# Kernel optimization log

Hardware: AMD Instinct MI355X
Metric: run time of the kernel (lower is better)

Reference implementation:

```python
import jax, jax.numpy as jnp
import numpy as np

EPS = 1e-5

def _layernorm(x, g, b):
    mu = jnp.mean(x, axis=-1, keepdims=True)
    var = jnp.mean(jnp.square(x - mu), axis=-1, keepdims=True)
    return (x - mu) * jax.lax.rsqrt(var + EPS) * g + b

def _orthogonal(key, out_dim, in_dim):
    a = jax.random.normal(key, (max(out_dim, in_dim), min(out_dim, in_dim)), dtype=jnp.float32)
    q, r = jnp.linalg.qr(a)
    q = q * jnp.sign(jnp.diagonal(r))
    if out_dim < in_dim:
        q = q.T
    return q  # [out_dim, in_dim]

def setup_inputs() -> dict:
    key = jax.random.key(0)
    ks = jax.random.split(key, 4)
    B, OBS, H1, H2, F = 262144, 512, 128, 128, 128
    obs = jax.random.normal(ks[0], (B, OBS), dtype=jnp.float32)
    return {
        "obs": obs,
        "w1": _orthogonal(ks[1], H1, OBS), "b1": jnp.zeros((H1,), jnp.float32),
        "g1": jnp.ones((H1,), jnp.float32), "be1": jnp.zeros((H1,), jnp.float32),
        "w2": _orthogonal(ks[2], H2, H1), "b2": jnp.zeros((H2,), jnp.float32),
        "g2": jnp.ones((H2,), jnp.float32), "be2": jnp.zeros((H2,), jnp.float32),
        "w3": _orthogonal(ks[3], F, H2), "b3": jnp.zeros((F,), jnp.float32),
    }

def reference(obs, w1, b1, g1, be1, w2, b2, g2, be2, w3, b3):
    x = jnp.tanh(_layernorm(obs @ w1.T + b1, g1, be1))
    x = jnp.tanh(_layernorm(x @ w2.T + b2, g2, be2))
    return jnp.tanh(x @ w3.T + b3)
```

## Files before the change

kernel.cpp:

```cpp
#include <hip/hip_runtime.h>
#include <hip/hip_bf16.h>

typedef __attribute__((ext_vector_type(8))) __bf16 bf16x8;
typedef __attribute__((ext_vector_type(4))) float f32x4;
typedef __attribute__((ext_vector_type(8))) float f32x8;

static __device__ __forceinline__ unsigned short bf16r(float f) {
  unsigned u = __builtin_bit_cast(unsigned, f);
  return (unsigned short)((u + 0x7FFFu + ((u >> 16) & 1u)) >> 16);
}

static __device__ __forceinline__ float ftanh(float x) {
  float e = __builtin_amdgcn_exp2f(x * 2.8853900817779268f);
  return 1.0f - 2.0f * __builtin_amdgcn_rcpf(e + 1.0f);
}

static __device__ __forceinline__ void gload_lds16(const void* g, void* l) {
  __builtin_amdgcn_global_load_lds(
      (const __attribute__((address_space(1))) unsigned int*)g,
      (__attribute__((address_space(3))) unsigned int*)l, 16, 0, 0);
}

__global__ void pack_kernel(const float* __restrict__ w1, const float* __restrict__ w2,
                            const float* __restrict__ w3, const float* __restrict__ b1,
                            const float* __restrict__ g1, const float* __restrict__ be1,
                            const float* __restrict__ b2, const float* __restrict__ g2,
                            const float* __restrict__ be2, const float* __restrict__ b3,
                            unsigned short* __restrict__ w1pk, unsigned short* __restrict__ w2pk,
                            unsigned short* __restrict__ w3pk, float* __restrict__ ppk) {
  int idx = blockIdx.x * 256 + threadIdx.x;
  if (idx < 65536) {
    int j = idx & 7, l = (idx >> 3) & 63, s = (idx >> 9) & 15, t = idx >> 13;
    int row = t * 16 + (l & 15);
    int col = s * 32 + (l >> 4) * 8 + j;
    w1pk[idx] = bf16r(w1[row * 512 + col]);
  } else if (idx < 81920) {
    int i = idx - 65536;
    int j = i & 7, l = (i >> 3) & 63, s = (i >> 9) & 3, t = i >> 11;
    int row = t * 16 + (l & 15);
    int col = (2 * s + (j >> 2)) * 16 + (l >> 4) * 4 + (j & 3);
    w2pk[i] = bf16r(w2[row * 128 + col]);
  } else if (idx < 98304) {
    int i = idx - 81920;
    int j = i & 7, l = (i >> 3) & 63, s = (i >> 9) & 3, t = i >> 11;
    int row = t * 16 + (l & 15);
    int col = (2 * s + (j >> 2)) * 16 + (l >> 4) * 4 + (j & 3);
    w3pk[i] = bf16r(w3[row * 128 + col]);
  } else if (idx < 99200) {
    int i = idx - 98304;
    int p = i >> 7;
    int r = i & 127;
    int qq = r >> 5, ii = r & 31;
    int m = (ii >> 2) * 16 + qq * 4 + (ii & 3);
    const float* src = (p == 0) ? b1 : (p == 1) ? g1 : (p == 2) ? be1
                     : (p == 3) ? b2 : (p == 4) ? g2 : (p == 5) ? be2 : b3;
    ppk[i] = src[m];
  }
}

__global__ __launch_bounds__(1024)
__attribute__((amdgpu_waves_per_eu(4, 4)))
void backbone_main(const float* __restrict__ obs,
                   const unsigned char* __restrict__ w1pk_g,
                   const bf16x8* __restrict__ w2pk,
                   const bf16x8* __restrict__ w3pk,
                   const float* __restrict__ ppk,
                   float* __restrict__ out) {
  __shared__ __align__(16) unsigned char lds[131072];

  const int tid  = threadIdx.x;
  const int lane = tid & 63;
  const int wv   = tid >> 6;
  const int q    = lane >> 4;
  const int rl   = lane & 15;
  const int l8   = lane >> 3;
  const int c8   = lane & 7;
  const unsigned rowR = blockIdx.x * 256 + wv * 16;
  const size_t brow = (size_t)rowR + (unsigned)rl;

  const unsigned char* gsrc = (const unsigned char*)obs
      + ((size_t)rowR + (unsigned)l8) * 2048 + (unsigned)((c8 ^ l8) * 16);
  unsigned char* obsS = lds + 65536 + wv * 4096;

  const unsigned rd0 = (unsigned)(rl * 128 + ((2 * q) ^ (rl & 7)) * 16);
  const unsigned rd1 = (unsigned)(rl * 128 + ((2 * q + 1) ^ (rl & 7)) * 16);

  gload_lds16(gsrc,                 obsS);
  gload_lds16(gsrc + 16384,         obsS + 1024);
  gload_lds16(gsrc + 128,           obsS + 2048);
  gload_lds16(gsrc + 128 + 16384,   obsS + 3072);
#pragma unroll
  for (int r = 0; r < 4; ++r) {
    unsigned o = r * 16384 + tid * 16;
    gload_lds16(w1pk_g + o + (o >> 13) * 8192, lds + r * 16384 + wv * 1024);
  }
  __syncthreads();

  const bf16x8* w1l = (const bf16x8*)lds;

  f32x4 acc[8];
#pragma unroll
  for (int t = 0; t < 8; ++t) acc[t] = (f32x4){0.f, 0.f, 0.f, 0.f};

#define KSTEP(s, WAITSTR)                                                        \
  {                                                                              \
    asm volatile("s_waitcnt " WAITSTR ::: "memory");                             \
    __builtin_amdgcn_sched_barrier(0);                                           \
    unsigned char* slot = obsS + ((s) & 1) * 2048;                               \
    f32x4 r0 = *(const f32x4*)(slot + rd0);                                      \
    f32x4 r1 = *(const f32x4*)(slot + rd1);                                      \
    asm volatile("s_waitcnt lgkmcnt(0)" ::: "memory");                           \
    __builtin_amdgcn_sched_barrier(0);                                           \
    if ((s) + 2 <= 15) {                                                         \
      gload_lds16(gsrc + ((s) + 2) * 128,         slot);                         \
      gload_lds16(gsrc + ((s) + 2) * 128 + 16384, slot + 1024);                  \
    }                                                                            \
    f32x8 rr = {r0.x, r0.y, r0.z, r0.w, r1.x, r1.y, r1.z, r1.w};                 \
    bf16x8 bfrag = __builtin_convertvector(rr, bf16x8);                          \
    _Pragma("unroll")                                                            \
    for (int t = 0; t < 8; ++t) {                                                \
      bf16x8 af = w1l[(t * 8 + ((s) & 7)) * 64 + lane];                          \
      acc[t] = __builtin_amdgcn_mfma_f32_16x16x32_bf16(af, bfrag, acc[t], 0, 0, 0); \
    }                                                                            \
  }

  KSTEP(0, "vmcnt(2)")
  KSTEP(1, "vmcnt(2)")
  KSTEP(2, "vmcnt(2)")
  KSTEP(3, "vmcnt(2)")
  KSTEP(4, "vmcnt(2)")
  KSTEP(5, "vmcnt(2)")
  KSTEP(6, "vmcnt(2)")
  KSTEP(7, "vmcnt(2)")

  __syncthreads();
#pragma unroll
  for (int r = 0; r < 4; ++r) {
    unsigned o = r * 16384 + tid * 16;
    gload_lds16(w1pk_g + o + ((o >> 13) + 1) * 8192, lds + r * 16384 + wv * 1024);
  }
  __syncthreads();

  KSTEP(8,  "vmcnt(2)")
  KSTEP(9,  "vmcnt(2)")
  KSTEP(10, "vmcnt(2)")
  KSTEP(11, "vmcnt(2)")
  KSTEP(12, "vmcnt(2)")
  KSTEP(13, "vmcnt(2)")
  KSTEP(14, "vmcnt(2)")
  KSTEP(15, "vmcnt(0)")
#undef KSTEP

  bf16x8 pkv[4];

  {
    const float* pb = ppk + 0 * 128 + q * 32;
    const float* pg = ppk + 1 * 128 + q * 32;
    const float* pe = ppk + 2 * 128 + q * 32;
    float s1 = 0.f, s2 = 0.f;
#pragma unroll
    for (int t = 0; t < 8; ++t) {
      f32x4 bb = *(const f32x4*)(pb + t * 4);
      f32x4 v = acc[t];
      v.x += bb.x; v.y += bb.y; v.z += bb.z; v.w += bb.w;
      acc[t] = v;
      s1 += (v.x + v.y) + (v.z + v.w);
      s2 += (v.x * v.x + v.y * v.y) + (v.z * v.z + v.w * v.w);
    }
    s1 += __shfl_xor(s1, 16, 64);
    s1 += __shfl_xor(s1, 32, 64);
    s2 += __shfl_xor(s2, 16, 64);
    s2 += __shfl_xor(s2, 32, 64);
    float mu  = s1 * (1.0f / 128.0f);
    float var = s2 * (1.0f / 128.0f) - mu * mu;
    float rs  = __builtin_amdgcn_rsqf(var + 1e-5f);
#pragma unroll
    for (int t2 = 0; t2 < 4; ++t2) {
      f32x4 ga = *(const f32x4*)(pg + (2 * t2) * 4);
      f32x4 gb = *(const f32x4*)(pg + (2 * t2 + 1) * 4);
      f32x4 ea = *(const f32x4*)(pe + (2 * t2) * 4);
      f32x4 eb = *(const f32x4*)(pe + (2 * t2 + 1) * 4);
      f32x4 va = acc[2 * t2];
      f32x4 vb = acc[2 * t2 + 1];
      f32x8 cat = {ftanh((va.x - mu) * rs * ga.x + ea.x),
                   ftanh((va.y - mu) * rs * ga.y + ea.y),
                   ftanh((va.z - mu) * rs * ga.z + ea.z),
                   ftanh((va.w - mu) * rs * ga.w + ea.w),
                   ftanh((vb.x - mu) * rs * gb.x + eb.x),
                   ftanh((vb.y - mu) * rs * gb.y + eb.y),
                   ftanh((vb.z - mu) * rs * gb.z + eb.z),
                   ftanh((vb.w - mu) * rs * gb.w + eb.w)};
      pkv[t2] = __builtin_convertvector(cat, bf16x8);
    }
  }

#pragma unroll
  for (int t = 0; t < 8; ++t) acc[t] = (f32x4){0.f, 0.f, 0.f, 0.f};
#pragma unroll
  for (int s = 0; s < 4; ++s) {
#pragma unroll
    for (int t = 0; t < 8; ++t) {
      bf16x8 af = w2pk[(t * 4 + s) * 64 + lane];
      acc[t] = __builtin_amdgcn_mfma_f32_16x16x32_bf16(af, pkv[s], acc[t], 0, 0, 0);
    }
  }

  {
    const float* pb = ppk + 3 * 128 + q * 32;
    const float* pg = ppk + 4 * 128 + q * 32;
    const float* pe = ppk + 5 * 128 + q * 32;
    float s1 = 0.f, s2 = 0.f;
#pragma unroll
    for (int t = 0; t < 8; ++t) {
      f32x4 bb = *(const f32x4*)(pb + t * 4);
      f32x4 v = acc[t];
      v.x += bb.x; v.y += bb.y; v.z += bb.z; v.w += bb.w;
      acc[t] = v;
      s1 += (v.x + v.y) + (v.z + v.w);
      s2 += (v.x * v.x + v.y * v.y) + (v.z * v.z + v.w * v.w);
    }
    s1 += __shfl_xor(s1, 16, 64);
    s1 += __shfl_xor(s1, 32, 64);
    s2 += __shfl_xor(s2, 16, 64);
    s2 += __shfl_xor(s2, 32, 64);
    float mu  = s1 * (1.0f / 128.0f);
    float var = s2 * (1.0f / 128.0f) - mu * mu;
    float rs  = __builtin_amdgcn_rsqf(var + 1e-5f);
#pragma unroll
    for (int t2 = 0; t2 < 4; ++t2) {
      f32x4 ga = *(const f32x4*)(pg + (2 * t2) * 4);
      f32x4 gb = *(const f32x4*)(pg + (2 * t2 + 1) * 4);
      f32x4 ea = *(const f32x4*)(pe + (2 * t2) * 4);
      f32x4 eb = *(const f32x4*)(pe + (2 * t2 + 1) * 4);
      f32x4 va = acc[2 * t2];
      f32x4 vb = acc[2 * t2 + 1];
      f32x8 cat = {ftanh((va.x - mu) * rs * ga.x + ea.x),
                   ftanh((va.y - mu) * rs * ga.y + ea.y),
                   ftanh((va.z - mu) * rs * ga.z + ea.z),
                   ftanh((va.w - mu) * rs * ga.w + ea.w),
                   ftanh((vb.x - mu) * rs * gb.x + eb.x),
                   ftanh((vb.y - mu) * rs * gb.y + eb.y),
                   ftanh((vb.z - mu) * rs * gb.z + eb.z),
                   ftanh((vb.w - mu) * rs * gb.w + eb.w)};
      pkv[t2] = __builtin_convertvector(cat, bf16x8);
    }
  }

#pragma unroll
  for (int t = 0; t < 8; ++t) acc[t] = (f32x4){0.f, 0.f, 0.f, 0.f};
#pragma unroll
  for (int s = 0; s < 4; ++s) {
#pragma unroll
    for (int t = 0; t < 8; ++t) {
      bf16x8 af = w3pk[(t * 4 + s) * 64 + lane];
      acc[t] = __builtin_amdgcn_mfma_f32_16x16x32_bf16(af, pkv[s], acc[t], 0, 0, 0);
    }
  }

  {
    const float* pb = ppk + 6 * 128 + q * 32;
    float* orow = out + brow * 128 + q * 4;
#pragma unroll
    for (int t = 0; t < 8; ++t) {
      f32x4 bb = *(const f32x4*)(pb + t * 4);
      f32x4 v = acc[t];
      f32x4 o = {ftanh(v.x + bb.x), ftanh(v.y + bb.y),
                 ftanh(v.z + bb.z), ftanh(v.w + bb.w)};
      __builtin_nontemporal_store(o, (f32x4*)(orow + t * 16));
    }
  }
}

extern "C" void kernel_launch(void* const* d_in, const int* in_sizes, int n_in,
                              void* d_out, int out_size, void* d_ws, size_t ws_size,
                              hipStream_t stream) {
  const float* obs = (const float*)d_in[0];
  const float* w1  = (const float*)d_in[1];
  const float* b1  = (const float*)d_in[2];
  const float* g1  = (const float*)d_in[3];
  const float* be1 = (const float*)d_in[4];
  const float* w2  = (const float*)d_in[5];
  const float* b2  = (const float*)d_in[6];
  const float* g2  = (const float*)d_in[7];
  const float* be2 = (const float*)d_in[8];
  const float* w3  = (const float*)d_in[9];
  const float* b3  = (const float*)d_in[10];

  unsigned short* w1pk = (unsigned short*)d_ws;
  unsigned short* w2pk = w1pk + 65536;
  unsigned short* w3pk = w2pk + 16384;
  float*          ppk  = (float*)(w3pk + 16384);

  pack_kernel<<<388, 256, 0, stream>>>(w1, w2, w3, b1, g1, be1, b2, g2, be2, b3,
                                       w1pk, w2pk, w3pk, ppk);

  backbone_main<<<1024, 1024, 0, stream>>>(obs, (const unsigned char*)w1pk,
                                           (const bf16x8*)w2pk, (const bf16x8*)w3pk,
                                           ppk, (float*)d_out);
}
```

Baseline: 198.6 us.

## Keep full W1 resident in LDS and single-buffer obs K-steps

Measured after the change: 200.5 us. Within noise of the previous version (+1.0%).

```diff
diff --git a/kernel.cpp b/kernel.cpp
--- a/kernel.cpp
+++ b/kernel.cpp
@@ -66,7 +66,7 @@
                    const bf16x8* __restrict__ w3pk,
                    const float* __restrict__ ppk,
                    float* __restrict__ out) {
-  __shared__ __align__(16) unsigned char lds[131072];
+  __shared__ __align__(16) unsigned char lds[163840];
 
   const int tid  = threadIdx.x;
   const int lane = tid & 63;
@@ -80,19 +80,16 @@
 
   const unsigned char* gsrc = (const unsigned char*)obs
       + ((size_t)rowR + (unsigned)l8) * 2048 + (unsigned)((c8 ^ l8) * 16);
-  unsigned char* obsS = lds + 65536 + wv * 4096;
+  unsigned char* slot = lds + 131072 + wv * 2048;
 
   const unsigned rd0 = (unsigned)(rl * 128 + ((2 * q) ^ (rl & 7)) * 16);
   const unsigned rd1 = (unsigned)(rl * 128 + ((2 * q + 1) ^ (rl & 7)) * 16);
 
-  gload_lds16(gsrc,                 obsS);
-  gload_lds16(gsrc + 16384,         obsS + 1024);
-  gload_lds16(gsrc + 128,           obsS + 2048);
-  gload_lds16(gsrc + 128 + 16384,   obsS + 3072);
-#pragma unroll
-  for (int r = 0; r < 4; ++r) {
-    unsigned o = r * 16384 + tid * 16;
-    gload_lds16(w1pk_g + o + (o >> 13) * 8192, lds + r * 16384 + wv * 1024);
+  gload_lds16(gsrc,         slot);
+  gload_lds16(gsrc + 16384, slot + 1024);
+#pragma unroll
+  for (int r = 0; r < 8; ++r) {
+    gload_lds16(w1pk_g + r * 16384 + tid * 16, lds + r * 16384 + wv * 1024);
   }
   __syncthreads();
 
@@ -102,53 +99,31 @@
 #pragma unroll
   for (int t = 0; t < 8; ++t) acc[t] = (f32x4){0.f, 0.f, 0.f, 0.f};
 
-#define KSTEP(s, WAITSTR)                                                        \
+#define KSTEP(s)                                                                 \
   {                                                                              \
-    asm volatile("s_waitcnt " WAITSTR ::: "memory");                             \
+    asm volatile("s_waitcnt vmcnt(0)" ::: "memory");                             \
     __builtin_amdgcn_sched_barrier(0);                                           \
-    unsigned char* slot = obsS + ((s) & 1) * 2048;                               \
     f32x4 r0 = *(const f32x4*)(slot + rd0);                                      \
     f32x4 r1 = *(const f32x4*)(slot + rd1);                                      \
     asm volatile("s_waitcnt lgkmcnt(0)" ::: "memory");                           \
     __builtin_amdgcn_sched_barrier(0);                                           \
-    if ((s) + 2 <= 15) {                                                         \
-      gload_lds16(gsrc + ((s) + 2) * 128,         slot);                         \
-      gload_lds16(gsrc + ((s) + 2) * 128 + 16384, slot + 1024);                  \
+    if ((s) < 15) {                                                              \
+      gload_lds16(gsrc + ((s) + 1) * 128,         slot);                         \
+      gload_lds16(gsrc + ((s) + 1) * 128 + 16384, slot + 1024);                  \
     }                                                                            \
     f32x8 rr = {r0.x, r0.y, r0.z, r0.w, r1.x, r1.y, r1.z, r1.w};                 \
     bf16x8 bfrag = __builtin_convertvector(rr, bf16x8);                          \
     _Pragma("unroll")                                                            \
     for (int t = 0; t < 8; ++t) {                                                \
-      bf16x8 af = w1l[(t * 8 + ((s) & 7)) * 64 + lane];                          \
+      bf16x8 af = w1l[(t * 16 + (s)) * 64 + lane];                               \
       acc[t] = __builtin_amdgcn_mfma_f32_16x16x32_bf16(af, bfrag, acc[t], 0, 0, 0); \
     }                                                                            \
   }
 
-  KSTEP(0, "vmcnt(2)")
-  KSTEP(1, "vmcnt(2)")
-  KSTEP(2, "vmcnt(2)")
-  KSTEP(3, "vmcnt(2)")
-  KSTEP(4, "vmcnt(2)")
-  KSTEP(5, "vmcnt(2)")
-  KSTEP(6, "vmcnt(2)")
-  KSTEP(7, "vmcnt(2)")
-
-  __syncthreads();
-#pragma unroll
-  for (int r = 0; r < 4; ++r) {
-    unsigned o = r * 16384 + tid * 16;
-    gload_lds16(w1pk_g + o + ((o >> 13) + 1) * 8192, lds + r * 16384 + wv * 1024);
-  }
-  __syncthreads();
-
-  KSTEP(8,  "vmcnt(2)")
-  KSTEP(9,  "vmcnt(2)")
-  KSTEP(10, "vmcnt(2)")
-  KSTEP(11, "vmcnt(2)")
-  KSTEP(12, "vmcnt(2)")
-  KSTEP(13, "vmcnt(2)")
-  KSTEP(14, "vmcnt(2)")
-  KSTEP(15, "vmcnt(0)")
+  KSTEP(0)  KSTEP(1)  KSTEP(2)  KSTEP(3)
+  KSTEP(4)  KSTEP(5)  KSTEP(6)  KSTEP(7)
+  KSTEP(8)  KSTEP(9)  KSTEP(10) KSTEP(11)
+  KSTEP(12) KSTEP(13) KSTEP(14) KSTEP(15)
 #undef KSTEP
 
   bf16x8 pkv[4];
```
